# Kernel optimization log

Measured on AMD Instinct MI355X. Metric: run time of the kernel, lower is better.

## Reference

```python
import jax, jax.numpy as jnp
import numpy as np

B, S, H, FFN, E = 2, 2048, 1024, 4096, 8

def setup_inputs() -> dict:
    key = jax.random.key(0)
    k0, k1, k2, k3 = jax.random.split(key, 4)
    return {
        "hidden_states": jax.random.normal(k0, (B, S, H), dtype=jnp.float32),
        "Wr": jax.random.normal(k1, (H, E), dtype=jnp.float32) * 0.02,
        "br": jnp.zeros((E,), dtype=jnp.float32),
        "W1": jax.random.normal(k2, (E, H, FFN), dtype=jnp.float32) * 0.02,
        "W2": jax.random.normal(k3, (E, FFN, H), dtype=jnp.float32) * 0.02,
    }

def reference(hidden_states, Wr, br, W1, W2):
    b, s, h = hidden_states.shape
    x = hidden_states.reshape(-1, h)                      # [T, H]
    # sinkhorn routing branch in forward: sigmoid activation then top-1
    route = jax.nn.sigmoid(x @ Wr + br)                   # [T, E]
    max_prob = jnp.max(route, axis=1, keepdims=True)      # [T, 1]
    max_ind = jnp.argmax(route, axis=1)                   # [T] int
    out = jnp.zeros_like(x)
    n_experts = Wr.shape[1]
    for e in range(n_experts):  # small fixed expert set
        mask = (max_ind == e)[:, None].astype(x.dtype)    # [T, 1] dispatch mask
        # expert MLP: fc2(gelu(fc1(x))), no bias (add_bias_linear=False)
        y = jax.nn.gelu(x @ W1[e], approximate=False) @ W2[e]  # [T, H]
        out = out + mask * y                              # scatter-combine
    out = out * max_prob                                  # scale by router prob
    return out.reshape(b, s, h)
```

## Files before the change

### kernel.cpp

```cpp
#include <hip/hip_runtime.h>
#include <hip/hip_bf16.h>
#include <math.h>

#define TOK 4096
#define HD 1024
#define FD 4096
#define NE 8

typedef __attribute__((ext_vector_type(4))) float f32x4;
typedef __attribute__((ext_vector_type(8))) short s16x8;
typedef __attribute__((ext_vector_type(4))) unsigned short u16x4;

__device__ __forceinline__ unsigned short f2bf(float f) {
    union { float f; unsigned u; } v; v.f = f;
    unsigned r = v.u + 0x7FFFu + ((v.u >> 16) & 1u);
    return (unsigned short)(r >> 16);
}

__global__ void router_kernel(const float* __restrict__ x, const float* __restrict__ Wr,
                              const float* __restrict__ br, int* __restrict__ counts,
                              int* __restrict__ tlist, float* __restrict__ mprob) {
    const int lane = threadIdx.x & 63;
    const int t = blockIdx.x * 4 + (threadIdx.x >> 6);
    const float* xr = x + (size_t)t * HD;
    float acc[NE];
#pragma unroll
    for (int e = 0; e < NE; ++e) acc[e] = 0.f;
    for (int h = lane; h < HD; h += 64) {
        float xv = xr[h];
        f32x4 w0 = *(const f32x4*)(Wr + h * NE);
        f32x4 w1 = *(const f32x4*)(Wr + h * NE + 4);
        acc[0] += xv * w0.x; acc[1] += xv * w0.y; acc[2] += xv * w0.z; acc[3] += xv * w0.w;
        acc[4] += xv * w1.x; acc[5] += xv * w1.y; acc[6] += xv * w1.z; acc[7] += xv * w1.w;
    }
#pragma unroll
    for (int off = 32; off >= 1; off >>= 1)
#pragma unroll
        for (int e = 0; e < NE; ++e) acc[e] += __shfl_down(acc[e], off, 64);
    if (lane == 0) {
        float best = -1.f; int bi = 0;
#pragma unroll
        for (int e = 0; e < NE; ++e) {
            float r = 1.f / (1.f + expf(-(acc[e] + br[e])));
            if (r > best) { best = r; bi = e; }
        }
        mprob[t] = best;
        int pos = atomicAdd(&counts[bi], 1);
        tlist[bi * TOK + pos] = t;
    }
}

template<int KDIM, bool FC1>
__global__ __launch_bounds__(256, 2)
void expert_gemm(const float* __restrict__ Xf, const unsigned short* __restrict__ Ab,
                 const float* __restrict__ W, const int* __restrict__ counts,
                 const int* __restrict__ tlist, const float* __restrict__ mprob,
                 unsigned short* __restrict__ inter, float* __restrict__ out) {
    constexpr int NDIM = FC1 ? FD : HD;
    const int e = blockIdx.z;
    const int cnt = counts[e];
    const int m0 = blockIdx.y * 128;
    if (m0 >= cnt) return;
    const int n0 = blockIdx.x * 128;
    const float* We = W + (size_t)e * KDIM * NDIM;

    __shared__ unsigned short Al[128 * 64];
    __shared__ unsigned short Bl[128 * 64];
    __shared__ int s_tok[128];
    __shared__ float s_prob[128];

    const int tid = threadIdx.x;
    if (tid < 128) {
        int m = m0 + tid;
        int tk = (m < cnt) ? tlist[e * TOK + m] : -1;
        s_tok[tid] = tk;
        s_prob[tid] = (!FC1 && tk >= 0) ? mprob[tk] : 0.f;
    }
    __syncthreads();

    const int lane = tid & 63;
    const int wave = tid >> 6;
    const int wrow = (wave >> 1) << 6;
    const int wcol = (wave & 1) << 6;
    const int lm = lane & 15, quad = lane >> 4;

    f32x4 acc[4][4] = {};

    for (int k0 = 0; k0 < KDIM; k0 += 64) {
        if constexpr (FC1) {
#pragma unroll
            for (int it = 0; it < 8; ++it) {
                int q = tid + it * 256;
                int m = q >> 4;
                int kk = (q & 15) << 2;
                int tk = s_tok[m];
                f32x4 v = {};
                if (tk >= 0) v = *(const f32x4*)(Xf + (size_t)tk * KDIM + (k0 + kk));
                u16x4 pv;
                pv.x = f2bf(v.x); pv.y = f2bf(v.y); pv.z = f2bf(v.z); pv.w = f2bf(v.w);
                int pos = (m << 6) + (((((kk >> 3) + m) & 7) << 3) | (kk & 7));
                *(u16x4*)&Al[pos] = pv;
            }
        } else {
#pragma unroll
            for (int it = 0; it < 4; ++it) {
                int q = tid + it * 256;
                int m = q >> 3;
                int kg = q & 7;
                int tk = s_tok[m];
                s16x8 v = {};
                if (tk >= 0) v = *(const s16x8*)(Ab + (size_t)tk * KDIM + (k0 + (kg << 3)));
                int pos = (m << 6) + (((kg + m) & 7) << 3);
                *(s16x8*)&Al[pos] = v;
            }
        }
        {
            int tg = tid >> 5;
            int l32 = tid & 31;
#pragma unroll
            for (int nh = 0; nh < 4; ++nh) {
                int n = (nh << 5) + l32;
                const float* wp = We + (size_t)(k0 + (tg << 3)) * NDIM + (n0 + n);
                s16x8 bv;
#pragma unroll
                for (int kk = 0; kk < 8; ++kk)
                    bv[kk] = (short)f2bf(wp[kk * NDIM]);
                int pos = (n << 6) + (((tg + n) & 7) << 3);
                *(s16x8*)&Bl[pos] = bv;
            }
        }
        __syncthreads();
#pragma unroll
        for (int kt = 0; kt < 2; ++kt) {
            s16x8 af[4], bf[4];
            int gk = (kt << 2) + quad;
#pragma unroll
            for (int mt = 0; mt < 4; ++mt) {
                int m = wrow + (mt << 4) + lm;
                af[mt] = *(const s16x8*)&Al[(m << 6) + (((gk + m) & 7) << 3)];
            }
#pragma unroll
            for (int nt = 0; nt < 4; ++nt) {
                int n = wcol + (nt << 4) + lm;
                bf[nt] = *(const s16x8*)&Bl[(n << 6) + (((gk + n) & 7) << 3)];
            }
#pragma unroll
            for (int mt = 0; mt < 4; ++mt)
#pragma unroll
                for (int nt = 0; nt < 4; ++nt)
                    acc[mt][nt] = __builtin_amdgcn_mfma_f32_16x16x32_bf16(
                        af[mt], bf[nt], acc[mt][nt], 0, 0, 0);
        }
        __syncthreads();
    }

#pragma unroll
    for (int mt = 0; mt < 4; ++mt) {
#pragma unroll
        for (int r = 0; r < 4; ++r) {
            int row = wrow + (mt << 4) + (quad << 2) + r;
            if (m0 + row >= cnt) continue;
            int tk = s_tok[row];
            int colb = n0 + wcol + lm;
            if constexpr (FC1) {
#pragma unroll
                for (int nt = 0; nt < 4; ++nt) {
                    float v = acc[mt][nt][r];
                    float g = 0.5f * v * (1.f + erff(v * 0.70710678f));
                    inter[(size_t)tk * FD + colb + (nt << 4)] = f2bf(g);
                }
            } else {
                float p = s_prob[row];
#pragma unroll
                for (int nt = 0; nt < 4; ++nt)
                    out[(size_t)tk * HD + colb + (nt << 4)] = acc[mt][nt][r] * p;
            }
        }
    }
}

extern "C" void kernel_launch(void* const* d_in, const int* in_sizes, int n_in,
                              void* d_out, int out_size, void* d_ws, size_t ws_size,
                              hipStream_t stream) {
    const float* x  = (const float*)d_in[0];
    const float* Wr = (const float*)d_in[1];
    const float* br = (const float*)d_in[2];
    const float* W1 = (const float*)d_in[3];
    const float* W2 = (const float*)d_in[4];
    float* out = (float*)d_out;

    char* ws = (char*)d_ws;
    int* counts  = (int*)ws;
    float* mprob = (float*)(ws + 256);
    int* tlist   = (int*)(ws + 256 + 16384);
    unsigned short* inter = (unsigned short*)(ws + 256 + 16384 + 131072);

    hipMemsetAsync(counts, 0, NE * sizeof(int), stream);
    router_kernel<<<TOK / 4, 256, 0, stream>>>(x, Wr, br, counts, tlist, mprob);
    expert_gemm<HD, true><<<dim3(FD / 128, TOK / 128, NE), 256, 0, stream>>>(
        x, nullptr, W1, counts, tlist, mprob, inter, nullptr);
    expert_gemm<FD, false><<<dim3(HD / 128, TOK / 128, NE), 256, 0, stream>>>(
        nullptr, inter, W2, counts, tlist, mprob, nullptr, out);
}
```

Baseline: 624.7 us.

## Pre-cast weights/activations to bf16 and use direct global-to-LDS loads

Adds a transpose+cast kernel that converts each expert weight matrix to K-major bf16 in workspace, and the router now also writes a bf16 copy of x. The expert GEMM then fills its LDS tiles with global_load_lds 16-byte copies using precomputed swizzled row pointers instead of per-element strided fp32 loads and conversions. Grid axes are swapped so M varies fastest, and occupancy is raised to 3 blocks. The cost is extra passes over the weights (about 128MB of fp32 read plus bf16 written per call) and no double buffering.

```diff
diff --git a/kernel.cpp b/kernel.cpp
--- a/kernel.cpp
+++ b/kernel.cpp
@@ -11,6 +11,9 @@
 typedef __attribute__((ext_vector_type(8))) short s16x8;
 typedef __attribute__((ext_vector_type(4))) unsigned short u16x4;
 
+typedef const __attribute__((address_space(1))) void g_void;
+typedef __attribute__((address_space(3))) void lds_void;
+
 __device__ __forceinline__ unsigned short f2bf(float f) {
     union { float f; unsigned u; } v; v.f = f;
     unsigned r = v.u + 0x7FFFu + ((v.u >> 16) & 1u);
@@ -19,15 +22,18 @@
 
 __global__ void router_kernel(const float* __restrict__ x, const float* __restrict__ Wr,
                               const float* __restrict__ br, int* __restrict__ counts,
-                              int* __restrict__ tlist, float* __restrict__ mprob) {
+                              int* __restrict__ tlist, float* __restrict__ mprob,
+                              unsigned short* __restrict__ xb) {
     const int lane = threadIdx.x & 63;
     const int t = blockIdx.x * 4 + (threadIdx.x >> 6);
     const float* xr = x + (size_t)t * HD;
+    unsigned short* xbr = xb + (size_t)t * HD;
     float acc[NE];
 #pragma unroll
     for (int e = 0; e < NE; ++e) acc[e] = 0.f;
     for (int h = lane; h < HD; h += 64) {
         float xv = xr[h];
+        xbr[h] = f2bf(xv);
         f32x4 w0 = *(const f32x4*)(Wr + h * NE);
         f32x4 w1 = *(const f32x4*)(Wr + h * NE + 4);
         acc[0] += xv * w0.x; acc[1] += xv * w0.y; acc[2] += xv * w0.z; acc[3] += xv * w0.w;
@@ -50,19 +56,49 @@
     }
 }
 
-template<int KDIM, bool FC1>
-__global__ __launch_bounds__(256, 2)
-void expert_gemm(const float* __restrict__ Xf, const unsigned short* __restrict__ Ab,
-                 const float* __restrict__ W, const int* __restrict__ counts,
-                 const int* __restrict__ tlist, const float* __restrict__ mprob,
+template<int K, int N>
+__global__ __launch_bounds__(256)
+void transpose_cast(const float* __restrict__ src, unsigned short* __restrict__ dst) {
+    __shared__ unsigned short T[64][72];
+    const int e = blockIdx.z;
+    const int n0 = blockIdx.x * 64;
+    const int k0 = blockIdx.y * 64;
+    const int tid = threadIdx.x;
+    {
+        int c4 = (tid & 15) << 2;
+#pragma unroll
+        for (int it = 0; it < 4; ++it) {
+            int r = (tid >> 4) + it * 16;
+            f32x4 v = *(const f32x4*)(src + ((size_t)e * K + k0 + r) * N + n0 + c4);
+            u16x4 p; p.x = f2bf(v.x); p.y = f2bf(v.y); p.z = f2bf(v.z); p.w = f2bf(v.w);
+            *(u16x4*)&T[r][c4] = p;
+        }
+    }
+    __syncthreads();
+    {
+        int c = tid >> 2;
+        int q = tid & 3;
+        s16x8 v0, v1;
+#pragma unroll
+        for (int j = 0; j < 8; ++j) { v0[j] = (short)T[q * 16 + j][c]; v1[j] = (short)T[q * 16 + 8 + j][c]; }
+        unsigned short* op = dst + ((size_t)e * N + n0 + c) * K + k0 + q * 16;
+        *(s16x8*)op = v0;
+        *(s16x8*)(op + 8) = v1;
+    }
+}
+
+template<int K, bool FC1>
+__global__ __launch_bounds__(256, 3)
+void expert_gemm(const unsigned short* __restrict__ Asrc, const unsigned short* __restrict__ Wt,
+                 const int* __restrict__ counts, const int* __restrict__ tlist,
+                 const float* __restrict__ mprob,
                  unsigned short* __restrict__ inter, float* __restrict__ out) {
     constexpr int NDIM = FC1 ? FD : HD;
     const int e = blockIdx.z;
     const int cnt = counts[e];
-    const int m0 = blockIdx.y * 128;
+    const int m0 = blockIdx.x * 128;
     if (m0 >= cnt) return;
-    const int n0 = blockIdx.x * 128;
-    const float* We = W + (size_t)e * KDIM * NDIM;
+    const int n0 = blockIdx.y * 128;
 
     __shared__ unsigned short Al[128 * 64];
     __shared__ unsigned short Bl[128 * 64];
@@ -76,58 +112,39 @@
         s_tok[tid] = tk;
         s_prob[tid] = (!FC1 && tk >= 0) ? mprob[tk] : 0.f;
     }
-    __syncthreads();
 
     const int lane = tid & 63;
     const int wave = tid >> 6;
+    const unsigned short* aptr[4];
+    const unsigned short* bptr[4];
+    {
+        int lr = lane >> 3, g = lane & 7;
+#pragma unroll
+        for (int it = 0; it < 4; ++it) {
+            int r = wave * 32 + it * 8 + lr;
+            int kg = (g - r) & 7;
+            int m = m0 + r;
+            int tk = (m < cnt) ? tlist[e * TOK + m] : 0;
+            aptr[it] = Asrc + (size_t)tk * K + kg * 8;
+            bptr[it] = Wt + ((size_t)e * NDIM + n0 + r) * K + kg * 8;
+        }
+    }
+
     const int wrow = (wave >> 1) << 6;
     const int wcol = (wave & 1) << 6;
     const int lm = lane & 15, quad = lane >> 4;
 
     f32x4 acc[4][4] = {};
 
-    for (int k0 = 0; k0 < KDIM; k0 += 64) {
-        if constexpr (FC1) {
-#pragma unroll
-            for (int it = 0; it < 8; ++it) {
-                int q = tid + it * 256;
-                int m = q >> 4;
-                int kk = (q & 15) << 2;
-                int tk = s_tok[m];
-                f32x4 v = {};
-                if (tk >= 0) v = *(const f32x4*)(Xf + (size_t)tk * KDIM + (k0 + kk));
-                u16x4 pv;
-                pv.x = f2bf(v.x); pv.y = f2bf(v.y); pv.z = f2bf(v.z); pv.w = f2bf(v.w);
-                int pos = (m << 6) + (((((kk >> 3) + m) & 7) << 3) | (kk & 7));
-                *(u16x4*)&Al[pos] = pv;
-            }
-        } else {
-#pragma unroll
-            for (int it = 0; it < 4; ++it) {
-                int q = tid + it * 256;
-                int m = q >> 3;
-                int kg = q & 7;
-                int tk = s_tok[m];
-                s16x8 v = {};
-                if (tk >= 0) v = *(const s16x8*)(Ab + (size_t)tk * KDIM + (k0 + (kg << 3)));
-                int pos = (m << 6) + (((kg + m) & 7) << 3);
-                *(s16x8*)&Al[pos] = v;
-            }
-        }
-        {
-            int tg = tid >> 5;
-            int l32 = tid & 31;
-#pragma unroll
-            for (int nh = 0; nh < 4; ++nh) {
-                int n = (nh << 5) + l32;
-                const float* wp = We + (size_t)(k0 + (tg << 3)) * NDIM + (n0 + n);
-                s16x8 bv;
-#pragma unroll
-                for (int kk = 0; kk < 8; ++kk)
-                    bv[kk] = (short)f2bf(wp[kk * NDIM]);
-                int pos = (n << 6) + (((tg + n) & 7) << 3);
-                *(s16x8*)&Bl[pos] = bv;
-            }
+    for (int k0 = 0; k0 < K; k0 += 64) {
+        __syncthreads();
+#pragma unroll
+        for (int it = 0; it < 4; ++it) {
+            __builtin_amdgcn_global_load_lds((g_void*)aptr[it],
+                (lds_void*)&Al[wave * 2048 + it * 512], 16, 0, 0);
+            __builtin_amdgcn_global_load_lds((g_void*)bptr[it],
+                (lds_void*)&Bl[wave * 2048 + it * 512], 16, 0, 0);
+            aptr[it] += 64; bptr[it] += 64;
         }
         __syncthreads();
 #pragma unroll
@@ -151,7 +168,6 @@
                     acc[mt][nt] = __builtin_amdgcn_mfma_f32_16x16x32_bf16(
                         af[mt], bf[nt], acc[mt][nt], 0, 0, 0);
         }
-        __syncthreads();
     }
 
 #pragma unroll
@@ -190,15 +206,21 @@
     float* out = (float*)d_out;
 
     char* ws = (char*)d_ws;
-    int* counts  = (int*)ws;
-    float* mprob = (float*)(ws + 256);
-    int* tlist   = (int*)(ws + 256 + 16384);
-    unsigned short* inter = (unsigned short*)(ws + 256 + 16384 + 131072);
+    int* counts           = (int*)ws;
+    float* mprob          = (float*)(ws + 256);
+    int* tlist            = (int*)(ws + 16640);
+    unsigned short* xb    = (unsigned short*)(ws + 147712);
+    unsigned short* inter = (unsigned short*)(ws + 8536320);
+    unsigned short* Wt    = (unsigned short*)(ws + 42090752);
 
     hipMemsetAsync(counts, 0, NE * sizeof(int), stream);
-    router_kernel<<<TOK / 4, 256, 0, stream>>>(x, Wr, br, counts, tlist, mprob);
-    expert_gemm<HD, true><<<dim3(FD / 128, TOK / 128, NE), 256, 0, stream>>>(
-        x, nullptr, W1, counts, tlist, mprob, inter, nullptr);
-    expert_gemm<FD, false><<<dim3(HD / 128, TOK / 128, NE), 256, 0, stream>>>(
-        nullptr, inter, W2, counts, tlist, mprob, nullptr, out);
-}
+    router_kernel<<<TOK / 4, 256, 0, stream>>>(x, Wr, br, counts, tlist, mprob, xb);
+
+    transpose_cast<HD, FD><<<dim3(FD / 64, HD / 64, NE), 256, 0, stream>>>(W1, Wt);
+    expert_gemm<HD, true><<<dim3(TOK / 128, FD / 128, NE), 256, 0, stream>>>(
+        xb, Wt, counts, tlist, mprob, inter, nullptr);
+
+    transpose_cast<FD, HD><<<dim3(HD / 64, FD / 64, NE), 256, 0, stream>>>(W2, Wt);
+    expert_gemm<FD, false><<<dim3(TOK / 128, HD / 128, NE), 256, 0, stream>>>(
+        inter, Wt, counts, tlist, mprob, nullptr, out);
+}
```

Measured after the change: 867.9 us. 1.39x slower.
